# Kernel tuning notes

Hardware: AMD Instinct MI355X
Metric: run time of the kernel (lower is better)

## Reference

```python
import jax, jax.numpy as jnp
import numpy as np

N_RAYS = 4096
NUM_STEPS = 768
MIN_NEAR_LIDAR = 0.01
LIDAR_MAX_DEPTH = 0.81
BOUND = 1.0
DENSITY_SCALE = 1.0
HID = 64
OUT_DIM = 2  # out_lidar_color_dim (intensity + raydrop)


def setup_inputs() -> dict:
    key = jax.random.key(0)
    ks = jax.random.split(key, 12)
    rays_o = jax.random.normal(ks[0], (N_RAYS, 3), jnp.float32) * 0.1
    rd = jax.random.normal(ks[1], (N_RAYS, 3), jnp.float32)
    rays_d = rd / jnp.linalg.norm(rd, axis=-1, keepdims=True)
    time = jax.random.uniform(ks[2], (N_RAYS, 1), jnp.float32)
    s = lambda fan: 1.0 / np.sqrt(fan)
    W1 = jax.random.normal(ks[3], (4, HID), jnp.float32) * s(4)
    b1 = jnp.zeros((HID,), jnp.float32)
    W2 = jax.random.normal(ks[4], (HID, HID), jnp.float32) * s(HID)
    b2 = jnp.zeros((HID,), jnp.float32)
    w_sig = jax.random.normal(ks[5], (HID, 1), jnp.float32) * s(HID)
    b_sig = jnp.zeros((1,), jnp.float32)
    Wc1 = jax.random.normal(ks[6], (3 + HID, HID), jnp.float32) * s(3 + HID)
    bc1 = jnp.zeros((HID,), jnp.float32)
    Wc2 = jax.random.normal(ks[7], (HID, OUT_DIM), jnp.float32) * s(HID)
    bc2 = jnp.zeros((OUT_DIM,), jnp.float32)
    return {"rays_o": rays_o, "rays_d": rays_d, "time": time,
            "W1": W1, "b1": b1, "W2": W2, "b2": b2,
            "w_sig": w_sig, "b_sig": b_sig,
            "Wc1": Wc1, "bc1": bc1, "Wc2": Wc2, "bc2": bc2}


def reference(rays_o, rays_d, time, W1, b1, W2, b2, w_sig, b_sig, Wc1, bc1, Wc2, bc2):
    N, S = rays_o.shape[0], NUM_STEPS
    nears = MIN_NEAR_LIDAR
    fars = LIDAR_MAX_DEPTH
    # stratified z values along each ray (no perturb)
    z = jnp.linspace(0.0, 1.0, S, dtype=rays_o.dtype)          # [S]
    z_vals = jnp.broadcast_to(nears + (fars - nears) * z, (N, S))
    sample_dist = (fars - nears) / S
    # sample points, clamped to AABB [-bound, bound]^3
    xyzs = rays_o[:, None, :] + rays_d[:, None, :] * z_vals[..., None]  # [N,S,3]
    xyzs = jnp.clip(xyzs, -BOUND, BOUND)
    # surrogate time-conditioned density field (NVSF 4D field)
    t = jnp.broadcast_to(time[:, None, :], (N, S, 1))
    h = jax.nn.relu(jnp.concatenate([xyzs, t], -1) @ W1 + b1)  # [N,S,HID]
    h = jax.nn.relu(h @ W2 + b2)
    sigma = jax.nn.softplus(h @ w_sig + b_sig)[..., 0]          # [N,S]
    # surrogate lidar color head (dir + geo features)
    dirs = jnp.broadcast_to(rays_d[:, None, :], (N, S, 3))
    c = jax.nn.relu(jnp.concatenate([dirs, h], -1) @ Wc1 + bc1)
    rgbs = jax.nn.sigmoid(c @ Wc2 + bc2)                        # [N,S,OUT_DIM]
    # alpha compositing
    deltas = z_vals[..., 1:] - z_vals[..., :-1]
    deltas = jnp.concatenate([deltas, jnp.full_like(deltas[..., :1], sample_dist)], -1)
    alphas = 1.0 - jnp.exp(-deltas * DENSITY_SCALE * sigma)     # [N,S]
    alphas_shifted = jnp.concatenate(
        [jnp.ones_like(alphas[..., :1]), 1.0 - alphas + 1e-15], -1)
    weights = alphas * jnp.cumprod(alphas_shifted, axis=-1)[..., :-1]
    weights_sum = jnp.sum(weights, axis=-1)                     # [N]
    depth = jnp.sum(weights * z_vals, axis=-1)                  # [N]
    image = jnp.sum(weights[..., None] * rgbs, axis=-2)         # [N,OUT_DIM]
    # lidar branch: no background compositing
    return depth, image, weights_sum, weights, z_vals
```

## Files before the change

kernel.cpp:

```cpp
#include <hip/hip_runtime.h>
#include <hip/hip_bf16.h>
#include <math.h>

#define NR 4096
#define NS 768

#define OFF_IMAGE   (NR)
#define OFF_WSUM    (NR*3)
#define OFF_WEIGHTS (NR*4)
#define OFF_ZVALS   (NR*4 + NR*NS)

typedef short bf16x8 __attribute__((ext_vector_type(8)));
typedef float f32x4  __attribute__((ext_vector_type(4)));

static __device__ __forceinline__ unsigned cvt_pk_bf16(float a, float b){
    unsigned r;
    asm("v_cvt_pk_bf16_f32 %0, %1, %2" : "=v"(r) : "v"(a), "v"(b));
    return r;
}
static __device__ __forceinline__ f32x4 zero4(){ f32x4 r = {0.f,0.f,0.f,0.f}; return r; }

__global__ __launch_bounds__(256, 2) void mlp_mfma_kernel(
    const float* __restrict__ rays_o, const float* __restrict__ rays_d,
    const float* __restrict__ timev,
    const float* __restrict__ W1, const float* __restrict__ b1,
    const float* __restrict__ W2, const float* __restrict__ b2,
    const float* __restrict__ w_sig, const float* __restrict__ b_sig,
    const float* __restrict__ Wc1, const float* __restrict__ bc1,
    const float* __restrict__ Wc2, const float* __restrict__ bc2,
    float* __restrict__ alpha_out,
    float* __restrict__ rgb_out)
{
    __shared__ __align__(16) unsigned bounce[4][2048];
    __shared__ __align__(16) unsigned stash[16*64*4];
    const int wid  = threadIdx.x >> 6;
    const int lane = threadIdx.x & 63;
    const int g = lane >> 4;
    const int c = lane & 15;

    if (wid == 0) {
        #pragma unroll
        for (int ft = 0; ft < 4; ++ft) {
            const int col = ft*16 + c;
            unsigned u0=0,u1=0,u2=0,u3=0, d0=0,d1=0;
            if (g == 0) {
                u0 = cvt_pk_bf16(W1[0*64+col], W1[1*64+col]);
                u1 = cvt_pk_bf16(W1[2*64+col], W1[3*64+col]);
                u2 = cvt_pk_bf16(b1[col], 0.f);
                d0 = cvt_pk_bf16(Wc1[0*64+col], Wc1[1*64+col]);
                d1 = cvt_pk_bf16(Wc1[2*64+col], bc1[col]);
            }
            unsigned* p = &stash[(ft*64 + lane)*4];
            p[0]=u0; p[1]=u1; p[2]=u2; p[3]=u3;
            unsigned* q = &stash[((4+ft)*64 + lane)*4];
            q[0]=d0; q[1]=d1; q[2]=0; q[3]=0;
        }
        #pragma unroll
        for (int kt = 0; kt < 2; ++kt) {
            unsigned s[4], w[4];
            #pragma unroll
            for (int p = 0; p < 4; ++p) {
                int k = kt*32 + 8*g + 2*p;
                s[p] = (c == 0) ? cvt_pk_bf16(w_sig[k], w_sig[k+1]) : 0u;
                w[p] = (c < 2)  ? cvt_pk_bf16(Wc2[k*2+c], Wc2[(k+1)*2+c]) : 0u;
            }
            unsigned* ps = &stash[((8+kt)*64 + lane)*4];
            ps[0]=s[0]; ps[1]=s[1]; ps[2]=s[2]; ps[3]=s[3];
            unsigned* pw = &stash[((10+kt)*64 + lane)*4];
            pw[0]=w[0]; pw[1]=w[1]; pw[2]=w[2]; pw[3]=w[3];
        }
        #pragma unroll
        for (int ft = 0; ft < 4; ++ft) {
            float* pb = reinterpret_cast<float*>(&stash[((12+ft)*64 + lane)*4]);
            #pragma unroll
            for (int r = 0; r < 4; ++r) pb[r] = b2[ft*16 + g*4 + r];
        }
    }

    auto ldfrag = [&](const float* __restrict__ W, int k0, int col)->bf16x8 {
        union { bf16x8 v; unsigned u[4]; } r;
        #pragma unroll
        for (int p = 0; p < 4; ++p) {
            int k = k0 + 2*p;
            r.u[p] = cvt_pk_bf16(W[k*64 + col], W[(k+1)*64 + col]);
        }
        return r.v;
    };
    bf16x8 bW2A[2][4], bWc1A[2][4];
    #pragma unroll
    for (int ft = 0; ft < 4; ++ft) {
        const int col = ft*16 + c;
        #pragma unroll
        for (int kt = 0; kt < 2; ++kt) {
            bW2A[kt][ft]  = ldfrag(W2,         kt*32 + 8*g, col);
            bWc1A[kt][ft] = ldfrag(Wc1 + 3*64, kt*32 + 8*g, col);
        }
    }
    const float bsg = b_sig[0];
    f32x4 bc2v;
    bc2v[0] = (g==0) ? bc2[0] : 0.f;
    bc2v[1] = (g==0) ? bc2[1] : 0.f;
    bc2v[2] = 0.f; bc2v[3] = 0.f;

    __syncthreads();

    unsigned* BW = &bounce[wid][0];
    const int wbase = c*8 + g*2;
    const int rbase = (g>>1)*128 + c*8 + (g&1)*4;
    auto SL = [&](int s)->bf16x8 {
        return *reinterpret_cast<const bf16x8*>(&stash[(s*64 + lane)*4]);
    };
    auto RD = [&](int kt, int nt)->bf16x8 {
        return *reinterpret_cast<const bf16x8*>(&BW[rbase + (nt*4 + kt*2)*128]);
    };

    const int gwave = blockIdx.x*4 + wid;

    #pragma unroll 1
    for (int tt = 0; tt < 6; ++tt) {
        const int tile = gwave*6 + tt;
        const int n  = tile / 12;
        const int s0 = (tile - n*12) * 64;
        const int s  = s0 + lane;

        const float z  = 0.01f + 0.8f * ((float)s * (1.0f/767.0f));
        const float ox = rays_o[3*n+0], oy = rays_o[3*n+1], oz = rays_o[3*n+2];
        const float dx = rays_d[3*n+0], dy = rays_d[3*n+1], dz = rays_d[3*n+2];
        const float tm = timev[n];

        const float px = fminf(fmaxf(fmaf(dx, z, ox), -1.f), 1.f);
        const float py = fminf(fmaxf(fmaf(dy, z, oy), -1.f), 1.f);
        const float pz = fminf(fmaxf(fmaf(dz, z, oz), -1.f), 1.f);
        const unsigned p01 = cvt_pk_bf16(px, py);
        const unsigned p23 = cvt_pk_bf16(pz, tm);

        f32x4 acc[4][4];

        {
            bf16x8 a1[4];
            #pragma unroll
            for (int ft = 0; ft < 4; ++ft) a1[ft] = SL(ft);
            #pragma unroll
            for (int nt = 0; nt < 4; ++nt) {
                unsigned q0 = (unsigned)__shfl((int)p01, nt*16 + c);
                unsigned q1 = (unsigned)__shfl((int)p23, nt*16 + c);
                union { bf16x8 v; unsigned u[4]; } b;
                b.u[0] = (g==0) ? q0 : 0u;
                b.u[1] = (g==0) ? q1 : 0u;
                b.u[2] = (g==0) ? 0x00003F80u : 0u;
                b.u[3] = 0u;
                #pragma unroll
                for (int ft = 0; ft < 4; ++ft)
                    acc[ft][nt] = __builtin_amdgcn_mfma_f32_16x16x32_bf16(
                        a1[ft], b.v, zero4(), 0, 0, 0);
            }
        }
        #pragma unroll
        for (int ft = 0; ft < 4; ++ft)
            #pragma unroll
            for (int nt = 0; nt < 4; ++nt) {
                unsigned pk0 = cvt_pk_bf16(fmaxf(acc[ft][nt][0],0.f), fmaxf(acc[ft][nt][1],0.f));
                unsigned pk1 = cvt_pk_bf16(fmaxf(acc[ft][nt][2],0.f), fmaxf(acc[ft][nt][3],0.f));
                *reinterpret_cast<uint2*>(&BW[wbase + (nt*4+ft)*128]) = make_uint2(pk0, pk1);
            }

        {
            f32x4 b2v[4];
            #pragma unroll
            for (int ft = 0; ft < 4; ++ft)
                b2v[ft] = *reinterpret_cast<const f32x4*>(&stash[((12+ft)*64 + lane)*4]);
            #pragma unroll
            for (int nt = 0; nt < 4; ++nt) {
                bf16x8 f0 = RD(0, nt), f1 = RD(1, nt);
                #pragma unroll
                for (int ft = 0; ft < 4; ++ft) {
                    f32x4 d = __builtin_amdgcn_mfma_f32_16x16x32_bf16(bW2A[0][ft], f0, b2v[ft], 0,0,0);
                    acc[ft][nt] = __builtin_amdgcn_mfma_f32_16x16x32_bf16(bW2A[1][ft], f1, d, 0,0,0);
                }
            }
        }
        #pragma unroll
        for (int ft = 0; ft < 4; ++ft)
            #pragma unroll
            for (int nt = 0; nt < 4; ++nt) {
                unsigned pk0 = cvt_pk_bf16(fmaxf(acc[ft][nt][0],0.f), fmaxf(acc[ft][nt][1],0.f));
                unsigned pk1 = cvt_pk_bf16(fmaxf(acc[ft][nt][2],0.f), fmaxf(acc[ft][nt][3],0.f));
                *reinterpret_cast<uint2*>(&BW[wbase + (nt*4+ft)*128]) = make_uint2(pk0, pk1);
            }

        f32x4 sigD[4];
        {
            bf16x8 ad[4];
            #pragma unroll
            for (int ft = 0; ft < 4; ++ft) ad[ft] = SL(4+ft);
            bf16x8 ws0 = SL(8), ws1 = SL(9);
            union { bf16x8 v; unsigned u[4]; } fd;
            fd.u[0] = (g==0) ? cvt_pk_bf16(dx, dy) : 0u;
            fd.u[1] = (g==0) ? cvt_pk_bf16(dz, 1.0f) : 0u;
            fd.u[2] = 0u; fd.u[3] = 0u;
            #pragma unroll
            for (int nt = 0; nt < 4; ++nt) {
                bf16x8 f0 = RD(0, nt), f1 = RD(1, nt);
                #pragma unroll
                for (int ft = 0; ft < 4; ++ft) {
                    f32x4 d = __builtin_amdgcn_mfma_f32_16x16x32_bf16(bWc1A[0][ft], f0, zero4(), 0,0,0);
                    d = __builtin_amdgcn_mfma_f32_16x16x32_bf16(bWc1A[1][ft], f1, d, 0,0,0);
                    acc[ft][nt] = __builtin_amdgcn_mfma_f32_16x16x32_bf16(ad[ft], fd.v, d, 0,0,0);
                }
                f32x4 sd = __builtin_amdgcn_mfma_f32_16x16x32_bf16(ws0, f0, zero4(), 0,0,0);
                sigD[nt] = __builtin_amdgcn_mfma_f32_16x16x32_bf16(ws1, f1, sd, 0,0,0);
            }
        }
        #pragma unroll
        for (int ft = 0; ft < 4; ++ft)
            #pragma unroll
            for (int nt = 0; nt < 4; ++nt) {
                unsigned pk0 = cvt_pk_bf16(fmaxf(acc[ft][nt][0],0.f), fmaxf(acc[ft][nt][1],0.f));
                unsigned pk1 = cvt_pk_bf16(fmaxf(acc[ft][nt][2],0.f), fmaxf(acc[ft][nt][3],0.f));
                *reinterpret_cast<uint2*>(&BW[wbase + (nt*4+ft)*128]) = make_uint2(pk0, pk1);
            }

        {
            float v0 = __shfl(sigD[0][0], c);
            float v1 = __shfl(sigD[1][0], c);
            float v2 = __shfl(sigD[2][0], c);
            float v3 = __shfl(sigD[3][0], c);
            float pre = (g==0) ? v0 : ((g==1) ? v1 : ((g==2) ? v2 : v3));
            pre += bsg;
            float sig = fmaxf(pre, 0.f) + __logf(1.f + __expf(-fabsf(pre)));
            float dl  = (s == NS-1) ? (0.8f/768.0f) : (0.8f/767.0f);
            alpha_out[tile*64 + lane] = 1.0f - __expf(-dl * sig);
        }

        {
            bf16x8 c20 = SL(10), c21 = SL(11);
            f32x4 rgbD[4];
            #pragma unroll
            for (int nt = 0; nt < 4; ++nt) {
                bf16x8 f0 = RD(0, nt), f1 = RD(1, nt);
                f32x4 d = __builtin_amdgcn_mfma_f32_16x16x32_bf16(c20, f0, bc2v, 0,0,0);
                rgbD[nt] = __builtin_amdgcn_mfma_f32_16x16x32_bf16(c21, f1, d, 0,0,0);
            }
            float a0 = __shfl(rgbD[0][0], c), b0 = __shfl(rgbD[0][1], c);
            float a1 = __shfl(rgbD[1][0], c), b1v_ = __shfl(rgbD[1][1], c);
            float a2 = __shfl(rgbD[2][0], c), b2_ = __shfl(rgbD[2][1], c);
            float a3 = __shfl(rgbD[3][0], c), b3 = __shfl(rgbD[3][1], c);
            float r0 = (g==0) ? a0 : ((g==1) ? a1 : ((g==2) ? a2 : a3));
            float r1 = (g==0) ? b0 : ((g==1) ? b1v_ : ((g==2) ? b2_ : b3));
            r0 = 1.0f / (1.0f + __expf(-r0));
            r1 = 1.0f / (1.0f + __expf(-r1));
            *reinterpret_cast<float2*>(&rgb_out[2*(tile*64 + lane)]) = make_float2(r0, r1);
        }
    }
}

__global__ __launch_bounds__(256) void composite_kernel(
    const float* __restrict__ rgb,
    float* __restrict__ out)
{
    int gtid = blockIdx.x * 256 + threadIdx.x;
    int ray  = gtid >> 6;
    int lane = threadIdx.x & 63;
    if (ray >= NR) return;

    float* __restrict__ depth_o = out;
    float* __restrict__ image_o = out + OFF_IMAGE;
    float* __restrict__ wsum_o  = out + OFF_WSUM;
    float* __restrict__ w_o     = out + OFF_WEIGHTS;
    float* __restrict__ z_o     = out + OFF_ZVALS;

    float T = 1.0f;
    float depth = 0.0f, wsum = 0.0f, im0 = 0.0f, im1 = 0.0f;

    for (int ch = 0; ch < NS/64; ++ch) {
        int s   = ch*64 + lane;
        int idx = ray*NS + s;
        float a  = w_o[idx];
        float zv = 0.01f + 0.8f * ((float)s * (1.0f/767.0f));
        float f  = 1.0f - a + 1e-15f;

        float p = f;
        #pragma unroll
        for (int off = 1; off < 64; off <<= 1) {
            float v = __shfl_up(p, off, 64);
            if (lane >= off) p *= v;
        }
        float excl = __shfl_up(p, 1, 64);
        if (lane == 0) excl = 1.0f;

        float wgt = a * T * excl;

        float r0 = rgb[2*idx + 0], r1 = rgb[2*idx + 1];
        depth = fmaf(wgt, zv, depth);
        wsum += wgt;
        im0   = fmaf(wgt, r0, im0);
        im1   = fmaf(wgt, r1, im1);

        w_o[idx] = wgt;
        z_o[idx] = zv;

        T *= __shfl(p, 63, 64);
    }

    #pragma unroll
    for (int off = 32; off >= 1; off >>= 1) {
        depth += __shfl_down(depth, off, 64);
        wsum  += __shfl_down(wsum , off, 64);
        im0   += __shfl_down(im0  , off, 64);
        im1   += __shfl_down(im1  , off, 64);
    }
    if (lane == 0) {
        depth_o[ray]      = depth;
        image_o[2*ray+0]  = im0;
        image_o[2*ray+1]  = im1;
        wsum_o[ray]       = wsum;
    }
}

extern "C" void kernel_launch(void* const* d_in, const int* in_sizes, int n_in,
                              void* d_out, int out_size, void* d_ws, size_t ws_size,
                              hipStream_t stream) {
    const float* rays_o = (const float*)d_in[0];
    const float* rays_d = (const float*)d_in[1];
    const float* timev  = (const float*)d_in[2];
    const float* W1     = (const float*)d_in[3];
    const float* b1     = (const float*)d_in[4];
    const float* W2     = (const float*)d_in[5];
    const float* b2     = (const float*)d_in[6];
    const float* w_sig  = (const float*)d_in[7];
    const float* b_sig  = (const float*)d_in[8];
    const float* Wc1    = (const float*)d_in[9];
    const float* bc1    = (const float*)d_in[10];
    const float* Wc2    = (const float*)d_in[11];
    const float* bc2    = (const float*)d_in[12];

    float* out   = (float*)d_out;
    float* alpha = out + OFF_WEIGHTS;
    float* rgb   = (float*)d_ws;

    dim3 blk(256);
    hipLaunchKernelGGL(mlp_mfma_kernel, dim3(2048), blk, 0, stream,
                       rays_o, rays_d, timev, W1, b1, W2, b2, w_sig, b_sig,
                       Wc1, bc1, Wc2, bc2, alpha, rgb);

    hipLaunchKernelGGL(composite_kernel, dim3((NR*64)/256), blk, 0, stream, rgb, out);
}
```

Before: 123.2 us.

## Pack RGB intermediates as bf16, use packed int16 ReLU, raise MFMA wave priority

The RGB intermediate buffer is now stored as packed bf16 pairs instead of two floats, halving that workspace traffic between the MLP and composite kernels. ReLU is applied after bf16 conversion with a single packed signed-int16 max instead of two float max ops. MFMA blocks are wrapped in s_setprio to favour matrix issue, and compiler memory fences are added around LDS writes. The bf16 storage of sigmoid outputs reduces the precision of the image values.

```diff
diff --git a/kernel.cpp b/kernel.cpp
--- a/kernel.cpp
+++ b/kernel.cpp
@@ -18,7 +18,16 @@
     asm("v_cvt_pk_bf16_f32 %0, %1, %2" : "=v"(r) : "v"(a), "v"(b));
     return r;
 }
+static __device__ __forceinline__ unsigned pk_relu_bf16x2(unsigned x){
+    unsigned r;
+    asm("v_pk_max_i16 %0, %1, 0" : "=v"(r) : "v"(x));
+    return r;
+}
+static __device__ __forceinline__ float bf2f(unsigned short h){
+    return __builtin_bit_cast(float, ((unsigned)h) << 16);
+}
 static __device__ __forceinline__ f32x4 zero4(){ f32x4 r = {0.f,0.f,0.f,0.f}; return r; }
+static __device__ __forceinline__ void ldsfence(){ asm volatile("" ::: "memory"); }
 
 __global__ __launch_bounds__(256, 2) void mlp_mfma_kernel(
     const float* __restrict__ rays_o, const float* __restrict__ rays_d,
@@ -29,7 +38,7 @@
     const float* __restrict__ Wc1, const float* __restrict__ bc1,
     const float* __restrict__ Wc2, const float* __restrict__ bc2,
     float* __restrict__ alpha_out,
-    float* __restrict__ rgb_out)
+    unsigned* __restrict__ rgb_out)
 {
     __shared__ __align__(16) unsigned bounce[4][2048];
     __shared__ __align__(16) unsigned stash[16*64*4];
@@ -140,6 +149,7 @@
             bf16x8 a1[4];
             #pragma unroll
             for (int ft = 0; ft < 4; ++ft) a1[ft] = SL(ft);
+            __builtin_amdgcn_s_setprio(1);
             #pragma unroll
             for (int nt = 0; nt < 4; ++nt) {
                 unsigned q0 = (unsigned)__shfl((int)p01, nt*16 + c);
@@ -154,21 +164,25 @@
                     acc[ft][nt] = __builtin_amdgcn_mfma_f32_16x16x32_bf16(
                         a1[ft], b.v, zero4(), 0, 0, 0);
             }
-        }
+            __builtin_amdgcn_s_setprio(0);
+        }
+        ldsfence();
         #pragma unroll
         for (int ft = 0; ft < 4; ++ft)
             #pragma unroll
             for (int nt = 0; nt < 4; ++nt) {
-                unsigned pk0 = cvt_pk_bf16(fmaxf(acc[ft][nt][0],0.f), fmaxf(acc[ft][nt][1],0.f));
-                unsigned pk1 = cvt_pk_bf16(fmaxf(acc[ft][nt][2],0.f), fmaxf(acc[ft][nt][3],0.f));
+                unsigned pk0 = pk_relu_bf16x2(cvt_pk_bf16(acc[ft][nt][0], acc[ft][nt][1]));
+                unsigned pk1 = pk_relu_bf16x2(cvt_pk_bf16(acc[ft][nt][2], acc[ft][nt][3]));
                 *reinterpret_cast<uint2*>(&BW[wbase + (nt*4+ft)*128]) = make_uint2(pk0, pk1);
             }
+        ldsfence();
 
         {
             f32x4 b2v[4];
             #pragma unroll
             for (int ft = 0; ft < 4; ++ft)
                 b2v[ft] = *reinterpret_cast<const f32x4*>(&stash[((12+ft)*64 + lane)*4]);
+            __builtin_amdgcn_s_setprio(1);
             #pragma unroll
             for (int nt = 0; nt < 4; ++nt) {
                 bf16x8 f0 = RD(0, nt), f1 = RD(1, nt);
@@ -178,15 +192,18 @@
                     acc[ft][nt] = __builtin_amdgcn_mfma_f32_16x16x32_bf16(bW2A[1][ft], f1, d, 0,0,0);
                 }
             }
-        }
+            __builtin_amdgcn_s_setprio(0);
+        }
+        ldsfence();
         #pragma unroll
         for (int ft = 0; ft < 4; ++ft)
             #pragma unroll
             for (int nt = 0; nt < 4; ++nt) {
-                unsigned pk0 = cvt_pk_bf16(fmaxf(acc[ft][nt][0],0.f), fmaxf(acc[ft][nt][1],0.f));
-                unsigned pk1 = cvt_pk_bf16(fmaxf(acc[ft][nt][2],0.f), fmaxf(acc[ft][nt][3],0.f));
+                unsigned pk0 = pk_relu_bf16x2(cvt_pk_bf16(acc[ft][nt][0], acc[ft][nt][1]));
+                unsigned pk1 = pk_relu_bf16x2(cvt_pk_bf16(acc[ft][nt][2], acc[ft][nt][3]));
                 *reinterpret_cast<uint2*>(&BW[wbase + (nt*4+ft)*128]) = make_uint2(pk0, pk1);
             }
+        ldsfence();
 
         f32x4 sigD[4];
         {
@@ -198,6 +215,7 @@
             fd.u[0] = (g==0) ? cvt_pk_bf16(dx, dy) : 0u;
             fd.u[1] = (g==0) ? cvt_pk_bf16(dz, 1.0f) : 0u;
             fd.u[2] = 0u; fd.u[3] = 0u;
+            __builtin_amdgcn_s_setprio(1);
             #pragma unroll
             for (int nt = 0; nt < 4; ++nt) {
                 bf16x8 f0 = RD(0, nt), f1 = RD(1, nt);
@@ -210,15 +228,18 @@
                 f32x4 sd = __builtin_amdgcn_mfma_f32_16x16x32_bf16(ws0, f0, zero4(), 0,0,0);
                 sigD[nt] = __builtin_amdgcn_mfma_f32_16x16x32_bf16(ws1, f1, sd, 0,0,0);
             }
-        }
+            __builtin_amdgcn_s_setprio(0);
+        }
+        ldsfence();
         #pragma unroll
         for (int ft = 0; ft < 4; ++ft)
             #pragma unroll
             for (int nt = 0; nt < 4; ++nt) {
-                unsigned pk0 = cvt_pk_bf16(fmaxf(acc[ft][nt][0],0.f), fmaxf(acc[ft][nt][1],0.f));
-                unsigned pk1 = cvt_pk_bf16(fmaxf(acc[ft][nt][2],0.f), fmaxf(acc[ft][nt][3],0.f));
+                unsigned pk0 = pk_relu_bf16x2(cvt_pk_bf16(acc[ft][nt][0], acc[ft][nt][1]));
+                unsigned pk1 = pk_relu_bf16x2(cvt_pk_bf16(acc[ft][nt][2], acc[ft][nt][3]));
                 *reinterpret_cast<uint2*>(&BW[wbase + (nt*4+ft)*128]) = make_uint2(pk0, pk1);
             }
+        ldsfence();
 
         {
             float v0 = __shfl(sigD[0][0], c);
@@ -235,12 +256,15 @@
         {
             bf16x8 c20 = SL(10), c21 = SL(11);
             f32x4 rgbD[4];
+            __builtin_amdgcn_s_setprio(1);
             #pragma unroll
             for (int nt = 0; nt < 4; ++nt) {
                 bf16x8 f0 = RD(0, nt), f1 = RD(1, nt);
                 f32x4 d = __builtin_amdgcn_mfma_f32_16x16x32_bf16(c20, f0, bc2v, 0,0,0);
                 rgbD[nt] = __builtin_amdgcn_mfma_f32_16x16x32_bf16(c21, f1, d, 0,0,0);
             }
+            __builtin_amdgcn_s_setprio(0);
+            ldsfence();
             float a0 = __shfl(rgbD[0][0], c), b0 = __shfl(rgbD[0][1], c);
             float a1 = __shfl(rgbD[1][0], c), b1v_ = __shfl(rgbD[1][1], c);
             float a2 = __shfl(rgbD[2][0], c), b2_ = __shfl(rgbD[2][1], c);
@@ -249,13 +273,13 @@
             float r1 = (g==0) ? b0 : ((g==1) ? b1v_ : ((g==2) ? b2_ : b3));
             r0 = 1.0f / (1.0f + __expf(-r0));
             r1 = 1.0f / (1.0f + __expf(-r1));
-            *reinterpret_cast<float2*>(&rgb_out[2*(tile*64 + lane)]) = make_float2(r0, r1);
+            rgb_out[tile*64 + lane] = cvt_pk_bf16(r0, r1);
         }
     }
 }
 
 __global__ __launch_bounds__(256) void composite_kernel(
-    const float* __restrict__ rgb,
+    const unsigned* __restrict__ rgb,
     float* __restrict__ out)
 {
     int gtid = blockIdx.x * 256 + threadIdx.x;
@@ -290,7 +314,9 @@
 
         float wgt = a * T * excl;
 
-        float r0 = rgb[2*idx + 0], r1 = rgb[2*idx + 1];
+        unsigned pv = rgb[idx];
+        float r0 = bf2f((unsigned short)(pv & 0xffffu));
+        float r1 = bf2f((unsigned short)(pv >> 16));
         depth = fmaf(wgt, zv, depth);
         wsum += wgt;
         im0   = fmaf(wgt, r0, im0);
@@ -334,9 +360,9 @@
     const float* Wc2    = (const float*)d_in[11];
     const float* bc2    = (const float*)d_in[12];
 
-    float* out   = (float*)d_out;
-    float* alpha = out + OFF_WEIGHTS;
-    float* rgb   = (float*)d_ws;
+    float* out     = (float*)d_out;
+    float* alpha   = out + OFF_WEIGHTS;
+    unsigned* rgb  = (unsigned*)d_ws;
 
     dim3 blk(256);
     hipLaunchKernelGGL(mlp_mfma_kernel, dim3(2048), blk, 0, stream,
```

After: 138.9 us. 12.7% more time.
